# Kernel tuning notes

Measured on AMD Instinct MI355X. Metric: run time of the kernel, lower is better.

Reference implementation:

```python
import jax, jax.numpy as jnp
import numpy as np

# Fano-plane triples defining octonion multiplication: e_a e_b = e_c (cyclic)
_TRIPLES = [(1, 2, 4), (2, 3, 5), (3, 4, 6), (4, 5, 7), (5, 6, 1), (6, 7, 2), (7, 1, 3)]


def _oct_structure():
    """S3[i,j,k] = sign s.t. e_i * e_j = s * e_k (zero otherwise)."""
    idx = np.zeros((8, 8), dtype=np.int32)
    sgn = np.zeros((8, 8), dtype=np.float32)
    for j in range(8):
        idx[0, j] = j; sgn[0, j] = 1.0
    for i in range(1, 8):
        idx[i, 0] = i; sgn[i, 0] = 1.0
        idx[i, i] = 0; sgn[i, i] = -1.0
    for a, b, c in _TRIPLES:
        for (p, q, r) in ((a, b, c), (b, c, a), (c, a, b)):
            idx[p, q] = r; sgn[p, q] = 1.0
            idx[q, p] = r; sgn[q, p] = -1.0
    S3 = np.zeros((8, 8, 8), dtype=np.float32)
    for i in range(8):
        for j in range(8):
            S3[i, j, idx[i, j]] = sgn[i, j]
    return jnp.asarray(S3)


def _oct_full(W, S3):
    """Fold octonion structure into a dense block matrix.

    W: [8, out8, in8] per-component weights. Effective map:
      y_k = sum_{i,j} S3[i,j,k] * W_i @ x_j  ->  M[k*out8:, j*in8:] = sum_i S3[i,j,k] W_i
    Returns [8*out8, 8*in8].
    """
    M = jnp.einsum('ijk,ion->kojn', S3, W)  # [8, out8, 8, in8]
    k8, o8, j8, n8 = M.shape
    return M.reshape(k8 * o8, j8 * n8)


def setup_inputs() -> dict:
    key = jax.random.key(0)
    ks = jax.random.split(key, 6)
    B, T, D = 8, 1024, 1024
    S = 2048  # d_state = n_embd * expand_factor
    x = jax.random.normal(ks[0], (B, T, D), dtype=jnp.float32)
    h_prev = jnp.zeros((B, S), dtype=jnp.float32)
    WA = jax.random.normal(ks[1], (8, S // 8, S // 8), dtype=jnp.float32) * float(1.0 / np.sqrt(S))
    WB = jax.random.normal(ks[2], (8, S // 8, D // 8), dtype=jnp.float32) * float(1.0 / np.sqrt(D))
    WC = jax.random.normal(ks[3], (8, D // 8, S // 8), dtype=jnp.float32) * float(1.0 / np.sqrt(S))
    Wdelta = jax.random.normal(ks[4], (S, D), dtype=jnp.float32) * float(1.0 / np.sqrt(D))
    delta_bias = jnp.full((S,), -2.0, dtype=jnp.float32)
    return dict(x=x, h_prev=h_prev, WA=WA, WB=WB, WC=WC, Wdelta=Wdelta, delta_bias=delta_bias)


def reference(x, h_prev, WA, WB, WC, Wdelta, delta_bias):
    S3 = _oct_structure()
    Af = _oct_full(WA, S3)  # [S, S]
    Bf = _oct_full(WB, S3)  # [S, D]
    Cf = _oct_full(WC, S3)  # [D, S]
    # Selective gate: sigmoid(x @ Wdelta^T + bias)  [B, T, S]
    delta = jax.nn.sigmoid(jnp.einsum('btd,sd->bts', x, Wdelta) + delta_bias)
    # Input injection precomputed for all timesteps (B is time-invariant)
    Bx = jnp.einsum('btd,sd->bts', x, Bf)  # [B, T, S]

    def step(h, inp):
        bx_t, d_t = inp  # [B, S], [B, S]
        h_new = (1.0 - d_t) * h + d_t * (h @ Af.T + bx_t)
        return h_new, h_new

    h_last, hs = jax.lax.scan(step, h_prev, (jnp.swapaxes(Bx, 0, 1), jnp.swapaxes(delta, 0, 1)))
    # Readout applied to the full state history at once: y[t] = C(h[t])
    y = jnp.einsum('tbs,ds->btd', hs, Cf)  # [B, T, D]
    return y, h_last
```

## Files before the change

kernel.cpp:

```cpp
#include <hip/hip_runtime.h>
#include <hip/hip_bf16.h>

#define T_STEPS 1024
#define OFF_AFT   0ull
#define OFF_GCAT  4194304ull
#define OFF_CFT   8388608ull
#define OFF_DELTA 10485760ull
#define OFF_BX    27262976ull
#define OFF_HS    44040192ull
#define OFF_HBUF  60817408ull

typedef short short8 __attribute__((ext_vector_type(8)));
typedef float f32x4 __attribute__((ext_vector_type(4)));

__device__ __forceinline__ void build_oct_tables(int tid, int (*Is)[8], float (*Sg)[8]) {
  if (tid < 64) {
    int i = tid >> 3, j = tid & 7;
    int k = 0; float s = 0.f;
    if (i == 0)      { k = j; s = 1.f; }
    else if (j == 0) { k = i; s = 1.f; }
    else if (i == j) { k = 0; s = -1.f; }
    else {
      const int T7[7][3] = {{1,2,4},{2,3,5},{3,4,6},{4,5,7},{5,6,1},{6,7,2},{7,1,3}};
      for (int t = 0; t < 7; ++t) {
        int a = T7[t][0], b = T7[t][1], c = T7[t][2];
        const int P[3][3] = {{a,b,c},{b,c,a},{c,a,b}};
        for (int r = 0; r < 3; ++r) {
          if (i == P[r][0] && j == P[r][1]) { k = P[r][2]; s = 1.f; }
          if (i == P[r][1] && j == P[r][0]) { k = P[r][2]; s = -1.f; }
        }
      }
    }
    Is[j][k] = i; Sg[j][k] = s;
  }
  __syncthreads();
}

__device__ __forceinline__ unsigned short bf16r(float x) {
  unsigned u = __float_as_uint(x);
  return (unsigned short)((u + 0x7FFFu + ((u >> 16) & 1u)) >> 16);
}

__global__ __launch_bounds__(256) void fold_Ab(const float* __restrict__ WA, unsigned short* __restrict__ AfB) {
  __shared__ int Is[8][8]; __shared__ float Sg[8][8];
  build_oct_tables(threadIdx.x, Is, Sg);
  int g8 = blockIdx.x * 256 + threadIdx.x;
  int sp = g8 >> 8;
  int s0 = (g8 & 255) * 8;
  int k8 = sp >> 8, o = sp & 255;
  int j8 = s0 >> 8, n = s0 & 255;
  int i = Is[j8][k8]; float sg = Sg[j8][k8];
  const float* src = WA + (size_t)i * 65536 + (size_t)o * 256 + n;
  float4 f0 = *(const float4*)(src);
  float4 f1 = *(const float4*)(src + 4);
  unsigned short v[8];
  v[0] = bf16r(sg * f0.x); v[1] = bf16r(sg * f0.y); v[2] = bf16r(sg * f0.z); v[3] = bf16r(sg * f0.w);
  v[4] = bf16r(sg * f1.x); v[5] = bf16r(sg * f1.y); v[6] = bf16r(sg * f1.z); v[7] = bf16r(sg * f1.w);
  *(short8*)(AfB + (size_t)g8 * 8) = *(short8*)v;
}

__global__ __launch_bounds__(256) void fold_GC(const float* __restrict__ Wd, const float* __restrict__ WB,
                                               float* __restrict__ Gcat) {
  __shared__ int Is[8][8]; __shared__ float Sg[8][8];
  build_oct_tables(threadIdx.x, Is, Sg);
  int g4 = blockIdx.x * 256 + threadIdx.x;
  int col = (g4 & 1023) * 4;
  int d = g4 >> 10;
  float4 v;
  if (col < 2048) {
    v.x = Wd[(size_t)(col + 0) * 1024 + d];
    v.y = Wd[(size_t)(col + 1) * 1024 + d];
    v.z = Wd[(size_t)(col + 2) * 1024 + d];
    v.w = Wd[(size_t)(col + 3) * 1024 + d];
  } else {
    int sp = col - 2048;
    int k = sp >> 8;
    int j = d >> 7, n = d & 127;
    int i = Is[j][k]; float sg = Sg[j][k];
    const float* wb = WB + (size_t)i * 32768 + n;
    v.x = sg * wb[(size_t)((sp + 0) & 255) * 128];
    v.y = sg * wb[(size_t)((sp + 1) & 255) * 128];
    v.z = sg * wb[(size_t)((sp + 2) & 255) * 128];
    v.w = sg * wb[(size_t)((sp + 3) & 255) * 128];
  }
  *(float4*)(Gcat + (size_t)g4 * 4) = v;
}

__global__ __launch_bounds__(256) void fold_C(const float* __restrict__ WC, float* __restrict__ CfT) {
  __shared__ int Is[8][8]; __shared__ float Sg[8][8];
  build_oct_tables(threadIdx.x, Is, Sg);
  int g4 = blockIdx.x * 256 + threadIdx.x;
  int d0 = (g4 & 255) * 4;
  int s  = g4 >> 8;
  int j = s >> 8, n = s & 255;
  int k = d0 >> 7;
  int i = Is[j][k]; float sg = Sg[j][k];
  const float* wc = WC + (size_t)i * 32768 + n;
  float4 v;
  v.x = sg * wc[(size_t)((d0 + 0) & 127) * 256];
  v.y = sg * wc[(size_t)((d0 + 1) & 127) * 256];
  v.z = sg * wc[(size_t)((d0 + 2) & 127) * 256];
  v.w = sg * wc[(size_t)((d0 + 3) & 127) * 256];
  *(float4*)(CfT + (size_t)g4 * 4) = v;
}

__global__ __launch_bounds__(256) void init_h(const float* __restrict__ h_prev, unsigned long long* __restrict__ hx) {
  int gid = blockIdx.x * 256 + threadIdx.x;
  if (gid < 8192) {
    int c = gid >> 6, within = gid & 63;
    int pr = within >> 3, b = within & 7;
    int s = c * 16 + pr * 2;
    unsigned pk = (unsigned)bf16r(h_prev[(size_t)b * 2048 + s])
                | ((unsigned)bf16r(h_prev[(size_t)b * 2048 + s + 1]) << 16);
    hx[gid] = ((unsigned long long)pk << 32) | 0ull;
  } else {
    hx[gid] = 0x00000000FFFFFFFFull;
  }
}

__global__ __launch_bounds__(256) void gemm_dbx(const float* __restrict__ X, const float* __restrict__ G,
                                                const float* __restrict__ bias,
                                                float* __restrict__ dlt, float* __restrict__ Bx) {
  __shared__ unsigned short Ah[128 * 40], Al[128 * 40];
  __shared__ unsigned short Bh[128 * 40], Bl[128 * 40];
  const int bn = blockIdx.x, bm = blockIdx.y;
  const int tid = threadIdx.x;
  const int lane = tid & 63;
  const int w = tid >> 6;
  const int wr = w >> 1, wc = w & 1;
  const int lr = lane & 15, lk = lane >> 4;

  f32x4 acc[4][4];
  #pragma unroll
  for (int a = 0; a < 4; ++a)
    #pragma unroll
    for (int b = 0; b < 4; ++b) acc[a][b] = (f32x4){0.f, 0.f, 0.f, 0.f};

  for (int kt = 0; kt < 1024; kt += 32) {
    {
      int row = tid >> 1, kh = tid & 1;
      const float* ar = X + (size_t)(bm * 128 + row) * 1024 + kt + kh * 16;
      float vv[16];
      #pragma unroll
      for (int q = 0; q < 4; ++q) {
        float4 f = *(const float4*)(ar + q * 4);
        vv[q * 4 + 0] = f.x; vv[q * 4 + 1] = f.y; vv[q * 4 + 2] = f.z; vv[q * 4 + 3] = f.w;
      }
      unsigned* ah32 = (unsigned*)Ah + row * 20 + kh * 8;
      unsigned* al32 = (unsigned*)Al + row * 20 + kh * 8;
      #pragma unroll
      for (int j = 0; j < 8; ++j) {
        unsigned short h0 = bf16r(vv[2 * j]), h1 = bf16r(vv[2 * j + 1]);
        float r0 = vv[2 * j]     - __uint_as_float((unsigned)h0 << 16);
        float r1 = vv[2 * j + 1] - __uint_as_float((unsigned)h1 << 16);
        ah32[j] = (unsigned)h0 | ((unsigned)h1 << 16);
        al32[j] = (unsigned)bf16r(r0) | ((unsigned)bf16r(r1) << 16);
      }
    }
    {
      int kr = tid >> 3, cg = tid & 7;
      const float* br = G + (size_t)(kt + kr) * 4096 + bn * 128 + cg * 16;
      #pragma unroll
      for (int q = 0; q < 4; ++q) {
        float4 f = *(const float4*)(br + q * 4);
        float vv[4] = {f.x, f.y, f.z, f.w};
        #pragma unroll
        for (int e = 0; e < 4; ++e) {
          int n = cg * 16 + q * 4 + e;
          unsigned short h = bf16r(vv[e]);
          float r = vv[e] - __uint_as_float((unsigned)h << 16);
          Bh[n * 40 + kr] = h;
          Bl[n * 40 + kr] = bf16r(r);
        }
      }
    }
    __syncthreads();
    short8 ah[4], al[4], bh[4], bl[4];
    #pragma unroll
    for (int f = 0; f < 4; ++f) {
      int ma = (wr * 64 + f * 16 + lr) * 40 + lk * 8;
      int nb = (wc * 64 + f * 16 + lr) * 40 + lk * 8;
      ah[f] = *(const short8*)(Ah + ma);
      al[f] = *(const short8*)(Al + ma);
      bh[f] = *(const short8*)(Bh + nb);
      bl[f] = *(const short8*)(Bl + nb);
    }
    #pragma unroll
    for (int fm = 0; fm < 4; ++fm)
      #pragma unroll
      for (int fn = 0; fn < 4; ++fn) {
        acc[fm][fn] = __builtin_amdgcn_mfma_f32_16x16x32_bf16(ah[fm], bh[fn], acc[fm][fn], 0, 0, 0);
        acc[fm][fn] = __builtin_amdgcn_mfma_f32_16x16x32_bf16(ah[fm], bl[fn], acc[fm][fn], 0, 0, 0);
        acc[fm][fn] = __builtin_amdgcn_mfma_f32_16x16x32_bf16(al[fm], bh[fn], acc[fm][fn], 0, 0, 0);
      }
    __syncthreads();
  }
  const bool isDelta = (bn < 16);
  #pragma unroll
  for (int fm = 0; fm < 4; ++fm) {
    #pragma unroll
    for (int rr = 0; rr < 4; ++rr) {
      int r = bm * 128 + wr * 64 + fm * 16 + lk * 4 + rr;
      int t = r & 1023, b = r >> 10;
      size_t base = ((size_t)t * 8 + b) * 2048;
      #pragma unroll
      for (int fn = 0; fn < 4; ++fn) {
        int n = bn * 128 + wc * 64 + fn * 16 + lr;
        float v = acc[fm][fn][rr];
        if (isDelta) {
          v += bias[n];
          v = 1.0f / (1.0f + expf(-v));
          dlt[base + n] = v;
        } else {
          Bx[base + (n - 2048)] = v;
        }
      }
    }
  }
}

__global__ __launch_bounds__(256) void gemm_y(const float* __restrict__ HS, const float* __restrict__ CfT,
                                              float* __restrict__ out) {
  __shared__ unsigned short As[128 * 40];
  __shared__ unsigned short Bs[128 * 40];
  const int bn = blockIdx.x, bm = blockIdx.y;
  const int tid = threadIdx.x;
  const int lane = tid & 63;
  const int w = tid >> 6;
  const int wr = w >> 1, wc = w & 1;
  const int lr = lane & 15, lk = lane >> 4;

  f32x4 acc[4][4];
  #pragma unroll
  for (int a = 0; a < 4; ++a)
    #pragma unroll
    for (int b = 0; b < 4; ++b) acc[a][b] = (f32x4){0.f, 0.f, 0.f, 0.f};

  for (int kt = 0; kt < 2048; kt += 32) {
    {
      int row = tid >> 1, kh = tid & 1;
      int rg = bm * 128 + row;
      const float* ar = HS + (size_t)((rg & 1023) * 8 + (rg >> 10)) * 2048 + kt + kh * 16;
      float vv[16];
      #pragma unroll
      for (int q = 0; q < 4; ++q) {
        float4 f = *(const float4*)(ar + q * 4);
        vv[q * 4 + 0] = f.x; vv[q * 4 + 1] = f.y; vv[q * 4 + 2] = f.z; vv[q * 4 + 3] = f.w;
      }
      unsigned* a32 = (unsigned*)As + row * 20 + kh * 8;
      #pragma unroll
      for (int j = 0; j < 8; ++j)
        a32[j] = (unsigned)bf16r(vv[2 * j]) | ((unsigned)bf16r(vv[2 * j + 1]) << 16);
    }
    {
      int kr = tid >> 3, cg = tid & 7;
      const float* br = CfT + (size_t)(kt + kr) * 1024 + bn * 128 + cg * 16;
      #pragma unroll
      for (int q = 0; q < 4; ++q) {
        float4 f = *(const float4*)(br + q * 4);
        float vv[4] = {f.x, f.y, f.z, f.w};
        #pragma unroll
        for (int e = 0; e < 4; ++e)
          Bs[(cg * 16 + q * 4 + e) * 40 + kr] = bf16r(vv[e]);
      }
    }
    __syncthreads();
    short8 aF[4], bF[4];
    #pragma unroll
    for (int f = 0; f < 4; ++f) {
      aF[f] = *(const short8*)(As + (wr * 64 + f * 16 + lr) * 40 + lk * 8);
      bF[f] = *(const short8*)(Bs + (wc * 64 + f * 16 + lr) * 40 + lk * 8);
    }
    #pragma unroll
    for (int fm = 0; fm < 4; ++fm)
      #pragma unroll
      for (int fn = 0; fn < 4; ++fn)
        acc[fm][fn] = __builtin_amdgcn_mfma_f32_16x16x32_bf16(aF[fm], bF[fn], acc[fm][fn], 0, 0, 0);
    __syncthreads();
  }
  #pragma unroll
  for (int fm = 0; fm < 4; ++fm)
    #pragma unroll
    for (int rr = 0; rr < 4; ++rr) {
      size_t rg = bm * 128 + wr * 64 + fm * 16 + lk * 4 + rr;
      #pragma unroll
      for (int fn = 0; fn < 4; ++fn) {
        int n = bn * 128 + wc * 64 + fn * 16 + lr;
        out[rg * 1024 + n] = acc[fm][fn][rr];
      }
    }
}

__global__ __launch_bounds__(512) void scan_kernel(const unsigned short* __restrict__ AfB,
                                                   const float* __restrict__ dlt,
                                                   const float* __restrict__ Bx, float* __restrict__ hs,
                                                   unsigned long long* __restrict__ hx,
                                                   const float* __restrict__ h_prev, float* __restrict__ hlast) {
  __shared__ float red[8 * 144];
  const int wg = blockIdx.x;
  const int tid = threadIdx.x;
  const int lane = tid & 63;
  const int w = tid >> 6;
  const int row = lane & 15;
  const int g4 = lane >> 4;
  const int nb = lane & 7;

  short8 afr[8];
  {
    const unsigned short* ab = AfB + (size_t)(wg * 16 + row) * 2048 + w * 256 + g4 * 8;
    #pragma unroll
    for (int q = 0; q < 8; ++q)
      afr[q] = *(const short8*)(ab + q * 32);
  }
  const int S0 = (g4 & 1) * 32 + nb;

  const int ub = tid >> 3, usp = (tid & 7) * 2;
  const int pword = wg * 64 + (tid & 7) * 8 + ub;
  float hr0 = 0.f, hr1 = 0.f;
  if (tid < 64) {
    hr0 = h_prev[(size_t)ub * 2048 + wg * 16 + usp];
    hr1 = h_prev[(size_t)ub * 2048 + wg * 16 + usp + 1];
  }

  #pragma unroll 1
  for (int t = 0; t < T_STEPS; ++t) {
    float2 dv = make_float2(0.f, 0.f), bxv = make_float2(0.f, 0.f);
    if (tid < 64) {
      size_t off = ((size_t)t * 8 + ub) * 2048 + wg * 16 + usp;
      dv  = *(const float2*)(dlt + off);
      bxv = *(const float2*)(Bx + off);
    }
    const unsigned want = (unsigned)t;
    const unsigned long long* bq = hx + (size_t)(t & 1) * 8192 + (size_t)w * 1024 + lane;
    unsigned long long wv[16];
    #pragma unroll
    for (int p = 0; p < 16; ++p)
      wv[p] = __hip_atomic_load(bq + p * 64, __ATOMIC_RELAXED, __HIP_MEMORY_SCOPE_SYSTEM);
    int fails = 0;
    for (;;) {
      bool stale = false;
      #pragma unroll
      for (int p = 0; p < 16; ++p) stale |= ((unsigned)wv[p] != want);
      if (!__any(stale)) break;
      if (++fails > 4) __builtin_amdgcn_s_sleep(1);
      #pragma unroll
      for (int p = 0; p < 16; ++p)
        if ((unsigned)wv[p] != want)
          wv[p] = __hip_atomic_load(bq + p * 64, __ATOMIC_RELAXED, __HIP_MEMORY_SCOPE_SYSTEM);
    }
    unsigned hi[16];
    #pragma unroll
    for (int p = 0; p < 16; ++p) hi[p] = (unsigned)(wv[p] >> 32);

    f32x4 acc = {0.f, 0.f, 0.f, 0.f};
    #pragma unroll
    for (int q = 0; q < 8; ++q) {
      union { unsigned d[4]; short8 v; } bb;
      #pragma unroll
      for (int u = 0; u < 4; ++u) {
        int S = S0 + u * 8;
        unsigned c0 = __shfl(hi[2 * q],     S, 64);
        unsigned c1 = __shfl(hi[2 * q + 1], S, 64);
        bb.d[u] = (g4 & 2) ? c1 : c0;
      }
      acc = __builtin_amdgcn_mfma_f32_16x16x32_bf16(afr[q], bb.v, acc, 0, 0, 0);
    }
    if (row < 8) {
      #pragma unroll
      for (int r = 0; r < 4; ++r)
        red[w * 144 + (g4 * 4 + r) * 9 + row] = acc[r];
    }
    __syncthreads();
    if (tid < 64) {
      float o0 = 0.f, o1 = 0.f;
      #pragma unroll
      for (int ww = 0; ww < 8; ++ww) {
        o0 += red[ww * 144 + usp * 9 + ub];
        o1 += red[ww * 144 + (usp + 1) * 9 + ub];
      }
      float h0 = fmaf(dv.x, o0 + bxv.x - hr0, hr0);
      float h1 = fmaf(dv.y, o1 + bxv.y - hr1, hr1);
      hr0 = h0; hr1 = h1;
      unsigned pk = (unsigned)bf16r(h0) | ((unsigned)bf16r(h1) << 16);
      unsigned long long wval = ((unsigned long long)pk << 32) | (unsigned long long)(unsigned)(t + 1);
      __hip_atomic_store(hx + (size_t)((t + 1) & 1) * 8192 + pword, wval,
                         __ATOMIC_RELAXED, __HIP_MEMORY_SCOPE_SYSTEM);
      size_t off = ((size_t)t * 8 + ub) * 2048 + wg * 16 + usp;
      *(float2*)(hs + off) = make_float2(h0, h1);
      if (t == T_STEPS - 1)
        *(float2*)(hlast + (size_t)ub * 2048 + wg * 16 + usp) = make_float2(h0, h1);
    }
    __syncthreads();
  }
}

extern "C" void kernel_launch(void* const* d_in, const int* in_sizes, int n_in,
                              void* d_out, int out_size, void* d_ws, size_t ws_size,
                              hipStream_t stream) {
  const float* x      = (const float*)d_in[0];
  const float* h_prev = (const float*)d_in[1];
  const float* WA     = (const float*)d_in[2];
  const float* WB     = (const float*)d_in[3];
  const float* WC     = (const float*)d_in[4];
  const float* Wd     = (const float*)d_in[5];
  const float* bias   = (const float*)d_in[6];
  float* out = (float*)d_out;
  float* w = (float*)d_ws;
  unsigned short* AfB = (unsigned short*)(w + OFF_AFT);
  float* Gcat = w + OFF_GCAT;
  float* CfT  = w + OFF_CFT;
  float* dlt  = w + OFF_DELTA;
  float* Bx   = w + OFF_BX;
  float* hs   = w + OFF_HS;
  unsigned long long* hx = (unsigned long long*)(w + OFF_HBUF);

  fold_Ab<<<2048, 256, 0, stream>>>(WA, AfB);
  fold_GC<<<4096, 256, 0, stream>>>(Wd, WB, Gcat);
  fold_C <<<2048, 256, 0, stream>>>(WC, CfT);
  init_h <<<64,   256, 0, stream>>>(h_prev, hx);
  gemm_dbx<<<dim3(32, 64), 256, 0, stream>>>(x, Gcat, bias, dlt, Bx);
  scan_kernel<<<128, 512, 0, stream>>>(AfB, dlt, Bx, hs, hx, h_prev, out + 8388608);
  gemm_y<<<dim3(8, 64), 256, 0, stream>>>(hs, CfT, out);
}
```

Baseline: 3.833 ms.

## Fuse delta/Bx GEMM into scan kernel with per-chunk readiness counters

Merges the delta/Bx projection GEMM and the recurrent scan into one launch. The first 128 blocks run the scan, and the remaining blocks compute GEMM tiles in time-chunk order, bumping a per-chunk counter when done. Scan blocks wait on the counter every 128 steps, so the scan can start before the whole GEMM is finished, hiding GEMM time behind the serial recurrence. It also switches GEMM tiles to 512 threads and raises wave priority around the critical h update. The risks are deadlock if the scan blocks are resident and GEMM blocks cannot get scheduled, and GEMM blocks contending with the latency-critical scan.

```diff
diff --git a/kernel.cpp b/kernel.cpp
--- a/kernel.cpp
+++ b/kernel.cpp
@@ -9,6 +9,7 @@
 #define OFF_BX    27262976ull
 #define OFF_HS    44040192ull
 #define OFF_HBUF  60817408ull
+#define OFF_CNT   60850176ull
 
 typedef short short8 __attribute__((ext_vector_type(8)));
 typedef float f32x4 __attribute__((ext_vector_type(4)));
@@ -104,7 +105,8 @@
   *(float4*)(CfT + (size_t)g4 * 4) = v;
 }
 
-__global__ __launch_bounds__(256) void init_h(const float* __restrict__ h_prev, unsigned long long* __restrict__ hx) {
+__global__ __launch_bounds__(256) void init_h(const float* __restrict__ h_prev, unsigned long long* __restrict__ hx,
+                                              int* __restrict__ cnt) {
   int gid = blockIdx.x * 256 + threadIdx.x;
   if (gid < 8192) {
     int c = gid >> 6, within = gid & 63;
@@ -116,106 +118,224 @@
   } else {
     hx[gid] = 0x00000000FFFFFFFFull;
   }
-}
-
-__global__ __launch_bounds__(256) void gemm_dbx(const float* __restrict__ X, const float* __restrict__ G,
-                                                const float* __restrict__ bias,
-                                                float* __restrict__ dlt, float* __restrict__ Bx) {
-  __shared__ unsigned short Ah[128 * 40], Al[128 * 40];
-  __shared__ unsigned short Bh[128 * 40], Bl[128 * 40];
-  const int bn = blockIdx.x, bm = blockIdx.y;
+  if (gid < 16) cnt[gid] = 0;
+}
+
+__global__ __launch_bounds__(512) void scan_dbx(const unsigned short* __restrict__ AfB,
+                                                float* __restrict__ dlt, float* __restrict__ Bx,
+                                                float* __restrict__ hs,
+                                                unsigned long long* __restrict__ hx,
+                                                const float* __restrict__ h_prev, float* __restrict__ hlast,
+                                                const float* __restrict__ X, const float* __restrict__ G,
+                                                const float* __restrict__ bias, int* __restrict__ chunkCnt) {
+  __shared__ __attribute__((aligned(16))) unsigned short Sm[4 * 128 * 40];
+  const int bid = blockIdx.x;
   const int tid = threadIdx.x;
   const int lane = tid & 63;
-  const int w = tid >> 6;
-  const int wr = w >> 1, wc = w & 1;
-  const int lr = lane & 15, lk = lane >> 4;
-
-  f32x4 acc[4][4];
-  #pragma unroll
-  for (int a = 0; a < 4; ++a)
-    #pragma unroll
-    for (int b = 0; b < 4; ++b) acc[a][b] = (f32x4){0.f, 0.f, 0.f, 0.f};
-
-  for (int kt = 0; kt < 1024; kt += 32) {
-    {
-      int row = tid >> 1, kh = tid & 1;
-      const float* ar = X + (size_t)(bm * 128 + row) * 1024 + kt + kh * 16;
-      float vv[16];
-      #pragma unroll
-      for (int q = 0; q < 4; ++q) {
-        float4 f = *(const float4*)(ar + q * 4);
-        vv[q * 4 + 0] = f.x; vv[q * 4 + 1] = f.y; vv[q * 4 + 2] = f.z; vv[q * 4 + 3] = f.w;
-      }
-      unsigned* ah32 = (unsigned*)Ah + row * 20 + kh * 8;
-      unsigned* al32 = (unsigned*)Al + row * 20 + kh * 8;
-      #pragma unroll
-      for (int j = 0; j < 8; ++j) {
-        unsigned short h0 = bf16r(vv[2 * j]), h1 = bf16r(vv[2 * j + 1]);
-        float r0 = vv[2 * j]     - __uint_as_float((unsigned)h0 << 16);
-        float r1 = vv[2 * j + 1] - __uint_as_float((unsigned)h1 << 16);
-        ah32[j] = (unsigned)h0 | ((unsigned)h1 << 16);
-        al32[j] = (unsigned)bf16r(r0) | ((unsigned)bf16r(r1) << 16);
-      }
-    }
-    {
-      int kr = tid >> 3, cg = tid & 7;
-      const float* br = G + (size_t)(kt + kr) * 4096 + bn * 128 + cg * 16;
-      #pragma unroll
-      for (int q = 0; q < 4; ++q) {
-        float4 f = *(const float4*)(br + q * 4);
-        float vv[4] = {f.x, f.y, f.z, f.w};
+
+  if (bid >= 128) {
+    const int gi = bid - 128;
+    const int bn = gi & 31;
+    const int bmSeq = gi >> 5;
+    const int ck = bmSeq >> 3, bb = bmSeq & 7;
+    const int bm = ck + 8 * bb;
+    unsigned short* Ah = Sm;
+    unsigned short* Al = Ah + 128 * 40;
+    unsigned short* Bh = Al + 128 * 40;
+    unsigned short* Bl = Bh + 128 * 40;
+    const int w8 = tid >> 6;
+    const int wr = w8 >> 2, wc = w8 & 3;
+    const int lr = lane & 15, lk = lane >> 4;
+
+    f32x4 acc[4][2];
+    #pragma unroll
+    for (int a = 0; a < 4; ++a) { acc[a][0] = (f32x4){0.f,0.f,0.f,0.f}; acc[a][1] = (f32x4){0.f,0.f,0.f,0.f}; }
+
+    for (int kt = 0; kt < 1024; kt += 32) {
+      {
+        int row = tid >> 2, kq = tid & 3;
+        const float* ar = X + (size_t)(bm * 128 + row) * 1024 + kt + kq * 8;
+        float4 f0 = *(const float4*)(ar);
+        float4 f1 = *(const float4*)(ar + 4);
+        float vv[8] = {f0.x, f0.y, f0.z, f0.w, f1.x, f1.y, f1.z, f1.w};
+        unsigned* ah32 = (unsigned*)Ah + row * 20 + kq * 4;
+        unsigned* al32 = (unsigned*)Al + row * 20 + kq * 4;
         #pragma unroll
-        for (int e = 0; e < 4; ++e) {
-          int n = cg * 16 + q * 4 + e;
+        for (int j = 0; j < 4; ++j) {
+          unsigned short h0 = bf16r(vv[2 * j]), h1 = bf16r(vv[2 * j + 1]);
+          float r0 = vv[2 * j]     - __uint_as_float((unsigned)h0 << 16);
+          float r1 = vv[2 * j + 1] - __uint_as_float((unsigned)h1 << 16);
+          ah32[j] = (unsigned)h0 | ((unsigned)h1 << 16);
+          al32[j] = (unsigned)bf16r(r0) | ((unsigned)bf16r(r1) << 16);
+        }
+      }
+      {
+        int kr = tid >> 4, cg = tid & 15;
+        const float* br = G + (size_t)(kt + kr) * 4096 + bn * 128 + cg * 8;
+        float4 f0 = *(const float4*)(br);
+        float4 f1 = *(const float4*)(br + 4);
+        float vv[8] = {f0.x, f0.y, f0.z, f0.w, f1.x, f1.y, f1.z, f1.w};
+        #pragma unroll
+        for (int e = 0; e < 8; ++e) {
+          int n = cg * 8 + e;
           unsigned short h = bf16r(vv[e]);
           float r = vv[e] - __uint_as_float((unsigned)h << 16);
           Bh[n * 40 + kr] = h;
           Bl[n * 40 + kr] = bf16r(r);
         }
       }
+      __syncthreads();
+      short8 ahf[4], alf[4], bhf[2], blf[2];
+      #pragma unroll
+      for (int f = 0; f < 4; ++f) {
+        int ma = (wr * 64 + f * 16 + lr) * 40 + lk * 8;
+        ahf[f] = *(const short8*)(Ah + ma);
+        alf[f] = *(const short8*)(Al + ma);
+      }
+      #pragma unroll
+      for (int e = 0; e < 2; ++e) {
+        int nb2 = (wc * 32 + e * 16 + lr) * 40 + lk * 8;
+        bhf[e] = *(const short8*)(Bh + nb2);
+        blf[e] = *(const short8*)(Bl + nb2);
+      }
+      #pragma unroll
+      for (int fm = 0; fm < 4; ++fm)
+        #pragma unroll
+        for (int fn = 0; fn < 2; ++fn) {
+          acc[fm][fn] = __builtin_amdgcn_mfma_f32_16x16x32_bf16(ahf[fm], bhf[fn], acc[fm][fn], 0, 0, 0);
+          acc[fm][fn] = __builtin_amdgcn_mfma_f32_16x16x32_bf16(ahf[fm], blf[fn], acc[fm][fn], 0, 0, 0);
+          acc[fm][fn] = __builtin_amdgcn_mfma_f32_16x16x32_bf16(alf[fm], bhf[fn], acc[fm][fn], 0, 0, 0);
+        }
+      __syncthreads();
+    }
+    const bool isDelta = (bn < 16);
+    #pragma unroll
+    for (int fm = 0; fm < 4; ++fm) {
+      #pragma unroll
+      for (int rr = 0; rr < 4; ++rr) {
+        int r = bm * 128 + wr * 64 + fm * 16 + lk * 4 + rr;
+        int t = r & 1023, b = r >> 10;
+        size_t base = ((size_t)t * 8 + b) * 2048;
+        #pragma unroll
+        for (int fn = 0; fn < 2; ++fn) {
+          int n = bn * 128 + wc * 32 + fn * 16 + lr;
+          float v = acc[fm][fn][rr];
+          if (isDelta) {
+            v += bias[n];
+            v = 1.0f / (1.0f + expf(-v));
+            __hip_atomic_store(&dlt[base + n], v, __ATOMIC_RELAXED, __HIP_MEMORY_SCOPE_SYSTEM);
+          } else {
+            __hip_atomic_store(&Bx[base + (n - 2048)], v, __ATOMIC_RELAXED, __HIP_MEMORY_SCOPE_SYSTEM);
+          }
+        }
+      }
     }
     __syncthreads();
-    short8 ah[4], al[4], bh[4], bl[4];
-    #pragma unroll
-    for (int f = 0; f < 4; ++f) {
-      int ma = (wr * 64 + f * 16 + lr) * 40 + lk * 8;
-      int nb = (wc * 64 + f * 16 + lr) * 40 + lk * 8;
-      ah[f] = *(const short8*)(Ah + ma);
-      al[f] = *(const short8*)(Al + ma);
-      bh[f] = *(const short8*)(Bh + nb);
-      bl[f] = *(const short8*)(Bl + nb);
-    }
-    #pragma unroll
-    for (int fm = 0; fm < 4; ++fm)
-      #pragma unroll
-      for (int fn = 0; fn < 4; ++fn) {
-        acc[fm][fn] = __builtin_amdgcn_mfma_f32_16x16x32_bf16(ah[fm], bh[fn], acc[fm][fn], 0, 0, 0);
-        acc[fm][fn] = __builtin_amdgcn_mfma_f32_16x16x32_bf16(ah[fm], bl[fn], acc[fm][fn], 0, 0, 0);
-        acc[fm][fn] = __builtin_amdgcn_mfma_f32_16x16x32_bf16(al[fm], bh[fn], acc[fm][fn], 0, 0, 0);
-      }
+    if (tid == 0)
+      __hip_atomic_fetch_add(&chunkCnt[ck], 1, __ATOMIC_RELAXED, __HIP_MEMORY_SCOPE_SYSTEM);
+    return;
+  }
+
+  float* red = (float*)Sm;
+  const int wg = bid;
+  const int w = tid >> 6;
+  const int row = lane & 15;
+  const int g4 = lane >> 4;
+  const int nb = lane & 7;
+
+  short8 afr[8];
+  {
+    const unsigned short* ab = AfB + (size_t)(wg * 16 + row) * 2048 + w * 256 + g4 * 8;
+    #pragma unroll
+    for (int q = 0; q < 8; ++q)
+      afr[q] = *(const short8*)(ab + q * 32);
+  }
+  const int S0 = (g4 & 1) * 32 + nb;
+
+  const int ub = tid >> 3, usp = (tid & 7) * 2;
+  const int pword = wg * 64 + (tid & 7) * 8 + ub;
+  float hr0 = 0.f, hr1 = 0.f;
+  if (tid < 64) {
+    hr0 = h_prev[(size_t)ub * 2048 + wg * 16 + usp];
+    hr1 = h_prev[(size_t)ub * 2048 + wg * 16 + usp + 1];
+  }
+
+  #pragma unroll 1
+  for (int t = 0; t < T_STEPS; ++t) {
+    float2 dv = make_float2(0.f, 0.f), bxv = make_float2(0.f, 0.f);
+    if (tid < 64) {
+      if ((t & 127) == 0) {
+        const int ck = t >> 7;
+        while (__hip_atomic_load(&chunkCnt[ck], __ATOMIC_RELAXED, __HIP_MEMORY_SCOPE_SYSTEM) < 256)
+          __builtin_amdgcn_s_sleep(16);
+      }
+      size_t off = ((size_t)t * 8 + ub) * 2048 + wg * 16 + usp;
+      dv  = *(const float2*)(dlt + off);
+      bxv = *(const float2*)(Bx + off);
+    }
+    const unsigned want = (unsigned)t;
+    const unsigned long long* bq = hx + (size_t)(t & 1) * 8192 + (size_t)w * 1024 + lane;
+    unsigned long long wv[16];
+    #pragma unroll
+    for (int p = 0; p < 16; ++p)
+      wv[p] = __hip_atomic_load(bq + p * 64, __ATOMIC_RELAXED, __HIP_MEMORY_SCOPE_SYSTEM);
+    int fails = 0;
+    for (;;) {
+      bool stale = false;
+      #pragma unroll
+      for (int p = 0; p < 16; ++p) stale |= ((unsigned)wv[p] != want);
+      if (!__any(stale)) break;
+      if (++fails > 4) __builtin_amdgcn_s_sleep(1);
+      #pragma unroll
+      for (int p = 0; p < 16; ++p)
+        if ((unsigned)wv[p] != want)
+          wv[p] = __hip_atomic_load(bq + p * 64, __ATOMIC_RELAXED, __HIP_MEMORY_SCOPE_SYSTEM);
+    }
+    unsigned hi[16];
+    #pragma unroll
+    for (int p = 0; p < 16; ++p) hi[p] = (unsigned)(wv[p] >> 32);
+
+    f32x4 acc = {0.f, 0.f, 0.f, 0.f};
+    #pragma unroll
+    for (int q = 0; q < 8; ++q) {
+      union { unsigned d[4]; short8 v; } bb;
+      #pragma unroll
+      for (int u = 0; u < 4; ++u) {
+        int S = S0 + u * 8;
+        unsigned c0 = __shfl(hi[2 * q],     S, 64);
+        unsigned c1 = __shfl(hi[2 * q + 1], S, 64);
+        bb.d[u] = (g4 & 2) ? c1 : c0;
+      }
+      acc = __builtin_amdgcn_mfma_f32_16x16x32_bf16(afr[q], bb.v, acc, 0, 0, 0);
+    }
+    if (row < 8) {
+      #pragma unroll
+      for (int r = 0; r < 4; ++r)
+        red[w * 144 + (g4 * 4 + r) * 9 + row] = acc[r];
+    }
     __syncthreads();
-  }
-  const bool isDelta = (bn < 16);
-  #pragma unroll
-  for (int fm = 0; fm < 4; ++fm) {
-    #pragma unroll
-    for (int rr = 0; rr < 4; ++rr) {
-      int r = bm * 128 + wr * 64 + fm * 16 + lk * 4 + rr;
-      int t = r & 1023, b = r >> 10;
-      size_t base = ((size_t)t * 8 + b) * 2048;
-      #pragma unroll
-      for (int fn = 0; fn < 4; ++fn) {
-        int n = bn * 128 + wc * 64 + fn * 16 + lr;
-        float v = acc[fm][fn][rr];
-        if (isDelta) {
-          v += bias[n];
-          v = 1.0f / (1.0f + expf(-v));
-          dlt[base + n] = v;
-        } else {
-          Bx[base + (n - 2048)] = v;
-        }
-      }
-    }
+    if (tid < 64) {
+      __builtin_amdgcn_s_setprio(1);
+      float o0 = 0.f, o1 = 0.f;
+      #pragma unroll
+      for (int ww = 0; ww < 8; ++ww) {
+        o0 += red[ww * 144 + usp * 9 + ub];
+        o1 += red[ww * 144 + (usp + 1) * 9 + ub];
+      }
+      float h0 = fmaf(dv.x, o0 + bxv.x - hr0, hr0);
+      float h1 = fmaf(dv.y, o1 + bxv.y - hr1, hr1);
+      hr0 = h0; hr1 = h1;
+      unsigned pk = (unsigned)bf16r(h0) | ((unsigned)bf16r(h1) << 16);
+      unsigned long long wval = ((unsigned long long)pk << 32) | (unsigned long long)(unsigned)(t + 1);
+      __hip_atomic_store(hx + (size_t)((t + 1) & 1) * 8192 + pword, wval,
+                         __ATOMIC_RELAXED, __HIP_MEMORY_SCOPE_SYSTEM);
+      __builtin_amdgcn_s_setprio(0);
+      size_t off = ((size_t)t * 8 + ub) * 2048 + wg * 16 + usp;
+      *(float2*)(hs + off) = make_float2(h0, h1);
+      if (t == T_STEPS - 1)
+        *(float2*)(hlast + (size_t)ub * 2048 + wg * 16 + usp) = make_float2(h0, h1);
+    }
+    __syncthreads();
   }
 }
 
@@ -289,109 +409,6 @@
         out[rg * 1024 + n] = acc[fm][fn][rr];
       }
     }
-}
-
-__global__ __launch_bounds__(512) void scan_kernel(const unsigned short* __restrict__ AfB,
-                                                   const float* __restrict__ dlt,
-                                                   const float* __restrict__ Bx, float* __restrict__ hs,
-                                                   unsigned long long* __restrict__ hx,
-                                                   const float* __restrict__ h_prev, float* __restrict__ hlast) {
-  __shared__ float red[8 * 144];
-  const int wg = blockIdx.x;
-  const int tid = threadIdx.x;
-  const int lane = tid & 63;
-  const int w = tid >> 6;
-  const int row = lane & 15;
-  const int g4 = lane >> 4;
-  const int nb = lane & 7;
-
-  short8 afr[8];
-  {
-    const unsigned short* ab = AfB + (size_t)(wg * 16 + row) * 2048 + w * 256 + g4 * 8;
-    #pragma unroll
-    for (int q = 0; q < 8; ++q)
-      afr[q] = *(const short8*)(ab + q * 32);
-  }
-  const int S0 = (g4 & 1) * 32 + nb;
-
-  const int ub = tid >> 3, usp = (tid & 7) * 2;
-  const int pword = wg * 64 + (tid & 7) * 8 + ub;
-  float hr0 = 0.f, hr1 = 0.f;
-  if (tid < 64) {
-    hr0 = h_prev[(size_t)ub * 2048 + wg * 16 + usp];
-    hr1 = h_prev[(size_t)ub * 2048 + wg * 16 + usp + 1];
-  }
-
-  #pragma unroll 1
-  for (int t = 0; t < T_STEPS; ++t) {
-    float2 dv = make_float2(0.f, 0.f), bxv = make_float2(0.f, 0.f);
-    if (tid < 64) {
-      size_t off = ((size_t)t * 8 + ub) * 2048 + wg * 16 + usp;
-      dv  = *(const float2*)(dlt + off);
-      bxv = *(const float2*)(Bx + off);
-    }
-    const unsigned want = (unsigned)t;
-    const unsigned long long* bq = hx + (size_t)(t & 1) * 8192 + (size_t)w * 1024 + lane;
-    unsigned long long wv[16];
-    #pragma unroll
-    for (int p = 0; p < 16; ++p)
-      wv[p] = __hip_atomic_load(bq + p * 64, __ATOMIC_RELAXED, __HIP_MEMORY_SCOPE_SYSTEM);
-    int fails = 0;
-    for (;;) {
-      bool stale = false;
-      #pragma unroll
-      for (int p = 0; p < 16; ++p) stale |= ((unsigned)wv[p] != want);
-      if (!__any(stale)) break;
-      if (++fails > 4) __builtin_amdgcn_s_sleep(1);
-      #pragma unroll
-      for (int p = 0; p < 16; ++p)
-        if ((unsigned)wv[p] != want)
-          wv[p] = __hip_atomic_load(bq + p * 64, __ATOMIC_RELAXED, __HIP_MEMORY_SCOPE_SYSTEM);
-    }
-    unsigned hi[16];
-    #pragma unroll
-    for (int p = 0; p < 16; ++p) hi[p] = (unsigned)(wv[p] >> 32);
-
-    f32x4 acc = {0.f, 0.f, 0.f, 0.f};
-    #pragma unroll
-    for (int q = 0; q < 8; ++q) {
-      union { unsigned d[4]; short8 v; } bb;
-      #pragma unroll
-      for (int u = 0; u < 4; ++u) {
-        int S = S0 + u * 8;
-        unsigned c0 = __shfl(hi[2 * q],     S, 64);
-        unsigned c1 = __shfl(hi[2 * q + 1], S, 64);
-        bb.d[u] = (g4 & 2) ? c1 : c0;
-      }
-      acc = __builtin_amdgcn_mfma_f32_16x16x32_bf16(afr[q], bb.v, acc, 0, 0, 0);
-    }
-    if (row < 8) {
-      #pragma unroll
-      for (int r = 0; r < 4; ++r)
-        red[w * 144 + (g4 * 4 + r) * 9 + row] = acc[r];
-    }
-    __syncthreads();
-    if (tid < 64) {
-      float o0 = 0.f, o1 = 0.f;
-      #pragma unroll
-      for (int ww = 0; ww < 8; ++ww) {
-        o0 += red[ww * 144 + usp * 9 + ub];
-        o1 += red[ww * 144 + (usp + 1) * 9 + ub];
-      }
-      float h0 = fmaf(dv.x, o0 + bxv.x - hr0, hr0);
-      float h1 = fmaf(dv.y, o1 + bxv.y - hr1, hr1);
-      hr0 = h0; hr1 = h1;
-      unsigned pk = (unsigned)bf16r(h0) | ((unsigned)bf16r(h1) << 16);
-      unsigned long long wval = ((unsigned long long)pk << 32) | (unsigned long long)(unsigned)(t + 1);
-      __hip_atomic_store(hx + (size_t)((t + 1) & 1) * 8192 + pword, wval,
-                         __ATOMIC_RELAXED, __HIP_MEMORY_SCOPE_SYSTEM);
-      size_t off = ((size_t)t * 8 + ub) * 2048 + wg * 16 + usp;
-      *(float2*)(hs + off) = make_float2(h0, h1);
-      if (t == T_STEPS - 1)
-        *(float2*)(hlast + (size_t)ub * 2048 + wg * 16 + usp) = make_float2(h0, h1);
-    }
-    __syncthreads();
-  }
 }
 
 extern "C" void kernel_launch(void* const* d_in, const int* in_sizes, int n_in,
@@ -413,12 +430,13 @@
   float* Bx   = w + OFF_BX;
   float* hs   = w + OFF_HS;
   unsigned long long* hx = (unsigned long long*)(w + OFF_HBUF);
+  int* chunkCnt = (int*)(w + OFF_CNT);
 
   fold_Ab<<<2048, 256, 0, stream>>>(WA, AfB);
   fold_GC<<<4096, 256, 0, stream>>>(Wd, WB, Gcat);
   fold_C <<<2048, 256, 0, stream>>>(WC, CfT);
-  init_h <<<64,   256, 0, stream>>>(h_prev, hx);
-  gemm_dbx<<<dim3(32, 64), 256, 0, stream>>>(x, Gcat, bias, dlt, Bx);
-  scan_kernel<<<128, 512, 0, stream>>>(AfB, dlt, Bx, hs, hx, h_prev, out + 8388608);
+  init_h <<<64,   256, 0, stream>>>(h_prev, hx, chunkCnt);
+  scan_dbx<<<2176, 512, 0, stream>>>(AfB, dlt, Bx, hs, hx, h_prev, out + 8388608,
+                                     x, Gcat, bias, chunkCnt);
   gemm_y<<<dim3(8, 64), 256, 0, stream>>>(hs, CfT, out);
 }
```

New measurement: 3.704 ms. 3.4% less time.
